# Performance work log

Measured on AMD Instinct MI355X. Metric: run time of the kernel, lower is better.

The kernel has to match this reference:

```python
import jax, jax.numpy as jnp
import numpy as np

C_IN = 144
PC = 288           # proj_channels = 2 * in_channels
HEADS = 12
DG = 12            # deformable groups
CLIP = 2
KH = KW = 3
A = KH * KW        # samples per clip per group (attention window 3x3)
PAD = 1
MAXMAG = 10.0
B, T, H, W = 1, 1, 64, 64


def _conv2d(x, w, b, pad):
    y = jax.lax.conv_general_dilated(x, w, (1, 1), [(pad, pad), (pad, pad)],
                                     dimension_numbers=('NCHW', 'OIHW', 'NCHW'))
    return y + b[None, :, None, None]


def _lrelu(x):
    return jnp.where(x >= 0, x, 0.1 * x)


def _linear_c(x, w, b):
    # per-pixel linear on channel dim; x: (..., Cin, h, w), w: (Cin, Cout)
    return jnp.einsum('...ihw,io->...ohw', x, w) + b[:, None, None]


def _bilinear_gather(feat, py, px):
    # feat: (b, clip, g, cg, h, w); py/px: (b, clip, g, A, h, w) absolute pixel coords
    # zero padding outside image (deformable-conv sampling semantics)
    b, cl, g, cg, h, w = feat.shape
    ff = feat.reshape(b, cl, g, cg, h * w)
    y0 = jnp.floor(py)
    x0 = jnp.floor(px)
    wy1 = py - y0
    wx1 = px - x0

    def corner(yc, xc, wt):
        valid = ((yc >= 0) & (yc < h) & (xc >= 0) & (xc < w)).astype(feat.dtype)
        yi = jnp.clip(yc, 0, h - 1).astype(jnp.int32)
        xi = jnp.clip(xc, 0, w - 1).astype(jnp.int32)
        idx = (yi * w + xi).reshape(b, cl, g, 1, -1)
        gat = jnp.take_along_axis(ff, idx, axis=-1).reshape(b, cl, g, cg, *py.shape[3:])
        return gat * (wt * valid)[:, :, :, None]

    out = corner(y0, x0, (1 - wy1) * (1 - wx1))
    out = out + corner(y0, x0 + 1, (1 - wy1) * wx1)
    out = out + corner(y0 + 1, x0, wy1 * (1 - wx1))
    out = out + corner(y0 + 1, x0 + 1, wy1 * wx1)
    return out  # (b, clip, g, cg, A, h, w)


def setup_inputs() -> dict:
    key = jax.random.key(0)
    ks = jax.random.split(key, 32)
    rn = lambda i, shp, s=1.0: jax.random.normal(ks[i], shp, dtype=jnp.float32) * s
    cin_off = C_IN * (1 + CLIP) + CLIP * 2   # 436
    c_off = CLIP * DG * A * 2                # 432
    d = {
        'q': rn(0, (B, T, C_IN, H, W)),
        'k': rn(1, (B, CLIP, C_IN, H, W)),
        'v': rn(2, (B, CLIP, C_IN, H, W)),
        'vpw0': rn(3, (B, T, C_IN, H, W)),
        'vpw1': rn(4, (B, T, C_IN, H, W)),
        'flow0': rn(5, (B, T, 2, H, W), 3.0),
        'flow1': rn(6, (B, T, 2, H, W), 3.0),
        'wo1': rn(7, (64, cin_off, 1, 1), 1.0 / np.sqrt(cin_off)),
        'bo1': rn(8, (64,), 0.01),
        'wo2': rn(9, (64, 64, 3, 3), 1.0 / np.sqrt(64 * 9)),
        'bo2': rn(10, (64,), 0.01),
        'wo3': rn(11, (64, 64, 3, 3), 1.0 / np.sqrt(64 * 9)),
        'bo3': rn(12, (64,), 0.01),
        'wo4': rn(13, (64, 64, 3, 3), 1.0 / np.sqrt(64 * 9)),
        'bo4': rn(14, (64,), 0.01),
        'wo5': rn(15, (64, 64, 3, 3), 1.0 / np.sqrt(64 * 9)),
        'bo5': rn(16, (64,), 0.01),
        'wo6': rn(17, (c_off, 64, 1, 1), 0.02),
        'bo6': rn(18, (c_off,), 0.01),
        'wq': rn(19, (C_IN, PC), 1.0 / np.sqrt(C_IN)),
        'bq': rn(20, (PC,), 0.01),
        'wk': rn(21, (C_IN, PC), 1.0 / np.sqrt(C_IN)),
        'bk': rn(22, (PC,), 0.01),
        'wv': rn(23, (C_IN, PC), 1.0 / np.sqrt(C_IN)),
        'bv': rn(24, (PC,), 0.01),
        'wp': rn(25, (PC, C_IN), 1.0 / np.sqrt(PC)),
        'bp': rn(26, (C_IN,), 0.01),
        'wm1': rn(27, (C_IN, 2 * C_IN), 1.0 / np.sqrt(C_IN)),
        'bm1': rn(28, (2 * C_IN,), 0.01),
        'wm2': rn(29, (2 * C_IN, C_IN), 1.0 / np.sqrt(2 * C_IN)),
        'bm2': rn(30, (C_IN,), 0.01),
    }
    return d


def reference(q, k, v, vpw0, vpw1, flow0, flow1,
              wo1, bo1, wo2, bo2, wo3, bo3, wo4, bo4, wo5, bo5, wo6, bo6,
              wq, bq, wk, bk, wv, bv, wp, bp, wm1, bm1, wm2, bm2):
    b, t, c, h, w = q.shape  # t == 1 here so q batch b*t matches kv batch b
    bt = b * t
    # --- offset predictor: Conv3d stack with time-kernel 1 == 2D convs ---
    x = jnp.concatenate([q, vpw0, vpw1, flow0, flow1], axis=2).reshape(bt, -1, h, w)
    x = _lrelu(_conv2d(x, wo1, bo1, 0))
    x = _lrelu(_conv2d(x, wo2, bo2, 1))
    x = _lrelu(_conv2d(x, wo3, bo3, 1))
    x = _lrelu(_conv2d(x, wo4, bo4, 1))
    x = _lrelu(_conv2d(x, wo5, bo5, 1))
    off = MAXMAG * jnp.tanh(_conv2d(x, wo6, bo6, 0))  # (bt, CLIP*DG*A*2, h, w)
    # add optical flow (channel-flipped to (y, x)) to every sample offset
    fyx = flow0.reshape(bt, 2, h, w)[:, ::-1]
    off = off + jnp.tile(fyx, (1, off.shape[1] // 2, 1, 1))
    off = off.reshape(bt, CLIP, DG, A, 2, h, w)
    ar = jnp.arange(A)
    by = (ar // KW - PAD).astype(q.dtype)  # kernel base offsets (stride=1, dil=1)
    bx = (ar % KW - PAD).astype(q.dtype)
    py = off[:, :, :, :, 0] + by[None, None, None, :, None, None] \
         + jnp.arange(h, dtype=q.dtype)[:, None]
    px = off[:, :, :, :, 1] + bx[None, None, None, :, None, None] \
         + jnp.arange(w, dtype=q.dtype)
    # --- q/k/v projections ---
    hd = PC // HEADS
    qp = _linear_c(q, wq, bq).reshape(bt, HEADS, hd, h, w)
    kp = _linear_c(k, wk, bk).reshape(b, CLIP, DG, PC // DG, h, w)
    vp = _linear_c(v, wv, bv).reshape(b, CLIP, DG, PC // DG, h, w)
    # --- deformable bilinear gather (per deformable group) ---
    ksamp = _bilinear_gather(kp, py, px).reshape(bt, CLIP, HEADS, hd, A, h, w)
    vsamp = _bilinear_gather(vp, py, px).reshape(bt, CLIP, HEADS, hd, A, h, w)
    # --- attention over CLIP*A sampled locations, per pixel per head ---
    scores = jnp.einsum('bmdyx,bcmdayx->bmcayx', qp, ksamp) * (hd ** -0.5)
    attn = jax.nn.softmax(scores.reshape(bt, HEADS, CLIP * A, h, w), axis=2)
    vflat = vsamp.transpose(0, 2, 1, 4, 3, 5, 6).reshape(bt, HEADS, CLIP * A, hd, h, w)
    out = jnp.einsum('bmsyx,bmsdyx->bmdyx', attn, vflat).reshape(b, t, PC, h, w)
    # --- output projection + MLP residual ---
    o = _linear_c(out, wp, bp)
    m = _linear_c(jax.nn.gelu(_linear_c(o, wm1, bm1), approximate=False), wm2, bm2)
    return o + m
```

## Files before the change

kernel.cpp:

```cpp
#include <hip/hip_runtime.h>
#include <hip/hip_bf16.h>
#include <math.h>

typedef __hip_bfloat16 bf16;
typedef __attribute__((ext_vector_type(8))) short bf16x8v;
typedef __attribute__((ext_vector_type(4))) float f32x4v;

#define NPIX 4096

__device__ __forceinline__ float b2f(bf16 v) { return __bfloat162float(v); }
__device__ __forceinline__ unsigned short f2bu(float f) {
    bf16 h = __float2bfloat16(f);
    return *(unsigned short*)&h;
}
__device__ __forceinline__ int detect_bf16(const unsigned short* __restrict__ qraw) {
    int lane = threadIdx.x & 63;
    unsigned short u = qraw[lane * 2];
    int e = (u >> 7) & 0xFF;
    unsigned long long ball = __ballot(e >= 100 && e <= 135);
    return __popcll(ball) > 32;
}

struct CArgs { const void* src[26]; int dstoff[26]; int n[26]; };

__global__ void convert_kernel(CArgs a, const unsigned short* __restrict__ qraw,
                               float* __restrict__ cw)
{
    const int isbf = detect_bf16(qraw);
    const int t = blockIdx.y;
    const int n = a.n[t];
    float* d = cw + a.dstoff[t];
    if (isbf) {
        const bf16* s = (const bf16*)a.src[t];
        for (int i = blockIdx.x * 256 + threadIdx.x; i < n; i += 256 * gridDim.x) d[i] = b2f(s[i]);
    } else {
        const float* s = (const float*)a.src[t];
        for (int i = blockIdx.x * 256 + threadIdx.x; i < n; i += 256 * gridDim.x) d[i] = s[i];
    }
}

struct PPJob { int dstS; int Mp, Kp, kr, mr, srcof, sstride, kind; };
struct PPArgs { PPJob j[11]; };

__global__ void prepack_kernel(PPArgs pa, const float* __restrict__ cw, short* __restrict__ wsS,
                               float* __restrict__ wsF)
{
    const int y = blockIdx.y;
    if (y < 11) {
        PPJob J = pa.j[y];
        const int tot = J.Mp * J.Kp;
        for (int e = blockIdx.x * 256 + threadIdx.x; e < tot; e += 256 * gridDim.x) {
            int m = e / J.Kp, k = e - m * J.Kp;
            float v = 0.f;
            if (J.kind == 0) { if (k < J.kr) v = cw[J.srcof + m * J.sstride + k]; }
            else             { if (k < J.kr && m < J.mr) v = cw[J.srcof + k * J.sstride + m]; }
            wsS[J.dstS + e] = (short)f2bu(v);
        }
    } else {
        const int OF_BP = 370512, OF_BM1 = 412128, OF_BM2 = 453888;
        for (int e = blockIdx.x * 256 + threadIdx.x; e < 576; e += 256 * gridDim.x) {
            if (e < 144)      wsF[5828544 + e] = cw[OF_BP + e];
            else if (e < 432) wsF[5828688 + e - 144] = cw[OF_BM1 + e - 144];
            else              wsF[5828976 + e - 432] = cw[OF_BM2 + e - 432];
        }
    }
}

__global__ void stage_pm_kernel(const void* __restrict__ s0, const void* __restrict__ s1,
                                const void* __restrict__ s2, const unsigned short* __restrict__ qraw,
                                short* __restrict__ xbase)
{
    const int isbf = detect_bf16(qraw);
    const int z = blockIdx.z;
    const int p = blockIdx.x * 256 + threadIdx.x;
    const int half = blockIdx.y;
    const void* srcs[5] = { s0, s1, s1, s2, s2 };
    const int clips[5] = { 0, 0, 1, 0, 1 };
    const size_t co = (size_t)clips[z] * 144 * NPIX;
    short* row = xbase + (size_t)z * 655360 + (size_t)p * 160;
    for (int c0 = half * 72; c0 < half * 72 + 72; c0 += 8) {
        unsigned short h[8];
        if (isbf) {
            const bf16* s = (const bf16*)srcs[z] + co;
#pragma unroll
            for (int i = 0; i < 8; ++i) h[i] = f2bu(b2f(s[(size_t)(c0 + i) * NPIX + p]));
        } else {
            const float* s = (const float*)srcs[z] + co;
#pragma unroll
            for (int i = 0; i < 8; ++i) h[i] = f2bu(s[(size_t)(c0 + i) * NPIX + p]);
        }
        uint4 u;
        u.x = (unsigned)h[0] | ((unsigned)h[1] << 16);
        u.y = (unsigned)h[2] | ((unsigned)h[3] << 16);
        u.z = (unsigned)h[4] | ((unsigned)h[5] << 16);
        u.w = (unsigned)h[6] | ((unsigned)h[7] << 16);
        *(uint4*)(row + c0) = u;
    }
    if (half == 1) {
        uint4 zz; zz.x = zz.y = zz.z = zz.w = 0u;
        *(uint4*)(row + 144) = zz;
        *(uint4*)(row + 152) = zz;
    }
}

__global__ void stage_x1_kernel(const void* __restrict__ q, const void* __restrict__ v0,
                                const void* __restrict__ v1, const float* __restrict__ cw,
                                const unsigned short* __restrict__ qraw, short* __restrict__ x1)
{
    const int isbf = detect_bf16(qraw);
    const int p = blockIdx.x * 256 + threadIdx.x;
    const int sec = blockIdx.y;
    short* row = x1 + (size_t)p * 448;
    if (sec < 3) {
        const void* srcs[3] = { q, v0, v1 };
        const int cbase = sec * 144;
        for (int c0 = 0; c0 < 144; c0 += 8) {
            unsigned short h[8];
            if (isbf) {
                const bf16* s = (const bf16*)srcs[sec];
#pragma unroll
                for (int i = 0; i < 8; ++i) h[i] = f2bu(b2f(s[(size_t)(c0 + i) * NPIX + p]));
            } else {
                const float* s = (const float*)srcs[sec];
#pragma unroll
                for (int i = 0; i < 8; ++i) h[i] = f2bu(s[(size_t)(c0 + i) * NPIX + p]);
            }
            uint4 u;
            u.x = (unsigned)h[0] | ((unsigned)h[1] << 16);
            u.y = (unsigned)h[2] | ((unsigned)h[3] << 16);
            u.z = (unsigned)h[4] | ((unsigned)h[5] << 16);
            u.w = (unsigned)h[6] | ((unsigned)h[7] << 16);
            *(uint4*)(row + cbase + c0) = u;
        }
    } else {
        const int OF_FL0 = 454032, OF_FL1 = 462224;
        unsigned short h[4];
        h[0] = f2bu(cw[OF_FL0 + p]);
        h[1] = f2bu(cw[OF_FL0 + NPIX + p]);
        h[2] = f2bu(cw[OF_FL1 + p]);
        h[3] = f2bu(cw[OF_FL1 + NPIX + p]);
        uint4 u;
        u.x = (unsigned)h[0] | ((unsigned)h[1] << 16);
        u.y = (unsigned)h[2] | ((unsigned)h[3] << 16);
        u.z = 0u; u.w = 0u;
        *(uint4*)(row + 432) = u;
        uint4 zz; zz.x = zz.y = zz.z = zz.w = 0u;
        *(uint4*)(row + 440) = zz;
    }
}

struct GemmDesc {
    const short* A; const short* B; const float* bias;
    void* dst; void* dst2; const unsigned short* qraw;
    int Mp, Kp, Mreal, mode, gofs;
};
struct GemmDesc5 { GemmDesc d[5]; };

template <int TM, int TN>
__global__ __launch_bounds__(256) void gemm_kernel(GemmDesc5 gd)
{
    const GemmDesc d = gd.d[blockIdx.z];
    const int wid = blockIdx.x * 4 + (threadIdx.x >> 6);
    const int lane = threadIdx.x & 63;
    const int tiles_m = d.Mp / (16 * TM);
    const int m0 = (wid % tiles_m) * (16 * TM);
    const int p0 = (wid / tiles_m) * (16 * TN);
    const int ar = lane & 15;
    const int kq = (lane >> 4) * 8;

    f32x4v acc[TM][TN];
#pragma unroll
    for (int i = 0; i < TM; ++i)
#pragma unroll
        for (int j = 0; j < TN; ++j) acc[i][j] = (f32x4v){0.f, 0.f, 0.f, 0.f};

    for (int k0 = 0; k0 < d.Kp; k0 += 32) {
        bf16x8v a[TM], b[TN];
#pragma unroll
        for (int i = 0; i < TM; ++i)
            a[i] = *(const bf16x8v*)(d.A + (size_t)(m0 + i * 16 + ar) * d.Kp + k0 + kq);
#pragma unroll
        for (int j = 0; j < TN; ++j)
            b[j] = *(const bf16x8v*)(d.B + (size_t)(p0 + j * 16 + ar) * d.Kp + k0 + kq);
#pragma unroll
        for (int i = 0; i < TM; ++i)
#pragma unroll
            for (int j = 0; j < TN; ++j)
                acc[i][j] = __builtin_amdgcn_mfma_f32_16x16x32_bf16(a[i], b[j], acc[i][j], 0, 0, 0);
    }

    const int isbf = (d.mode == 5) ? detect_bf16(d.qraw) : 0;
#pragma unroll
    for (int i = 0; i < TM; ++i) {
#pragma unroll
        for (int j = 0; j < TN; ++j) {
            const int pcol = p0 + j * 16 + (lane & 15);
#pragma unroll
            for (int r = 0; r < 4; ++r) {
                const int m = m0 + i * 16 + (lane >> 4) * 4 + r;
                float v = acc[i][j][r];
                if (m < d.Mreal) v += d.bias[m];
                if (d.mode == 0) {
                    v = (v >= 0.f) ? v : 0.1f * v;
                    ((unsigned short*)d.dst)[(size_t)pcol * d.Mp + m] = f2bu(v);
                } else if (d.mode == 1) {
                    int g = m / 24 + d.gofs;
                    ((unsigned short*)d.dst)[((size_t)g * NPIX + pcol) * 24 + (m % 24)] = f2bu(v);
                } else if (d.mode == 3) {
                    ((unsigned short*)d.dst)[(size_t)pcol * 160 + m] = f2bu(v);
                    if (m < 144) ((float*)d.dst2)[(size_t)pcol * 144 + m] = v;
                } else if (d.mode == 4) {
                    v = 0.5f * v * (1.f + erff(v * 0.70710678118654752f));
                    ((unsigned short*)d.dst)[(size_t)pcol * d.Mp + m] = f2bu(v);
                } else {
                    if (m < 144) {
                        v += ((float*)d.dst2)[(size_t)pcol * 144 + m];
                        if (isbf) ((unsigned short*)d.dst)[(size_t)m * NPIX + pcol] = f2bu(v);
                        else      ((float*)d.dst)[(size_t)m * NPIX + pcol] = v;
                    }
                }
            }
        }
    }
}

__device__ __forceinline__ unsigned short hw_get(const uint4& v, int idx) {
    unsigned w = (idx < 2) ? v.x : (idx < 4) ? v.y : (idx < 6) ? v.z : v.w;
    return (idx & 1) ? (unsigned short)(w >> 16) : (unsigned short)(w & 0xffff);
}

__global__ __launch_bounds__(256) void im2col_kernel(const short* __restrict__ Y,
                                                     short* __restrict__ B3)
{
    const int t = blockIdx.x * 256 + threadIdx.x;
    const int p = t >> 3;
    const int c0 = (t & 7) * 8;
    const int y = p >> 6, x = p & 63;
    uint4 v[9];
#pragma unroll
    for (int tap = 0; tap < 9; ++tap) {
        int yy = y + tap / 3 - 1, xx = x + tap % 3 - 1;
        int ok = ((unsigned)yy < 64u) & ((unsigned)xx < 64u);
        int idx = ok ? (yy * 64 + xx) : p;
        uint4 u = *(const uint4*)(Y + (size_t)idx * 64 + c0);
        if (!ok) { u.x = 0u; u.y = 0u; u.z = 0u; u.w = 0u; }
        v[tap] = u;
    }
    short* orow = B3 + (size_t)p * 576 + c0 * 9;
#pragma unroll
    for (int w = 0; w < 9; ++w) {
        unsigned short h[8];
#pragma unroll
        for (int s = 0; s < 8; ++s) {
            int e = w * 8 + s;
            h[s] = hw_get(v[e % 9], e / 9);
        }
        uint4 u;
        u.x = (unsigned)h[0] | ((unsigned)h[1] << 16);
        u.y = (unsigned)h[2] | ((unsigned)h[3] << 16);
        u.z = (unsigned)h[4] | ((unsigned)h[5] << 16);
        u.w = (unsigned)h[6] | ((unsigned)h[7] << 16);
        ((uint4*)orow)[w] = u;
    }
}

__global__ __launch_bounds__(256) void conv6_kernel(const short* __restrict__ YF,
                                                    const float* __restrict__ cw,
                                                    float* __restrict__ py, float* __restrict__ px)
{
    const int OF_WO6 = 175680, OF_BO6 = 203328, OF_FL0 = 454032;
    const int p = blockIdx.x * 256 + threadIdx.x;
    const int o0 = blockIdx.y * 16;
    const uint4* yrow = (const uint4*)(YF + (size_t)p * 64);
    const float* wb = cw + OF_WO6 + o0 * 64;

    float acc[16];
#pragma unroll
    for (int j = 0; j < 16; ++j) acc[j] = cw[OF_BO6 + o0 + j];

#pragma unroll
    for (int c = 0; c < 8; ++c) {
        uint4 u = yrow[c];
        float a0 = __uint_as_float(u.x << 16);
        float a1 = __uint_as_float(u.x & 0xFFFF0000u);
        float a2 = __uint_as_float(u.y << 16);
        float a3 = __uint_as_float(u.y & 0xFFFF0000u);
        float a4 = __uint_as_float(u.z << 16);
        float a5 = __uint_as_float(u.z & 0xFFFF0000u);
        float a6 = __uint_as_float(u.w << 16);
        float a7 = __uint_as_float(u.w & 0xFFFF0000u);
#pragma unroll
        for (int j = 0; j < 16; ++j) {
            const float* wr = wb + j * 64 + c * 8;
            acc[j] += a0 * wr[0] + a1 * wr[1] + a2 * wr[2] + a3 * wr[3]
                    + a4 * wr[4] + a5 * wr[5] + a6 * wr[6] + a7 * wr[7];
        }
    }

    const float f_y = cw[OF_FL0 + NPIX + p];
    const float f_x = cw[OF_FL0 + p];
    const float yf = (float)(p >> 6), xf = (float)(p & 63);
#pragma unroll
    for (int j = 0; j < 16; ++j) {
        int o = o0 + j;
        float val = 10.f * tanhf(acc[j]);
        int s = o >> 1;
        int a_idx = s % 9;
        if ((o & 1) == 0) py[s * NPIX + p] = val + f_y + (float)(a_idx / 3 - 1) + yf;
        else              px[s * NPIX + p] = val + f_x + (float)(a_idx % 3 - 1) + xf;
    }
}

__device__ __forceinline__ float dot12(const bf16* __restrict__ row, const float* qv) {
    const uint2* s = (const uint2*)row;
    float d = 0.f;
#pragma unroll
    for (int c = 0; c < 3; ++c) {
        uint2 u = s[c];
        d += qv[c * 4 + 0] * __uint_as_float(u.x << 16);
        d += qv[c * 4 + 1] * __uint_as_float(u.x & 0xFFFF0000u);
        d += qv[c * 4 + 2] * __uint_as_float(u.y << 16);
        d += qv[c * 4 + 3] * __uint_as_float(u.y & 0xFFFF0000u);
    }
    return d;
}
__device__ __forceinline__ void acc12(float* ov, const bf16* __restrict__ row, float f) {
    const uint2* s = (const uint2*)row;
#pragma unroll
    for (int c = 0; c < 3; ++c) {
        uint2 u = s[c];
        ov[c * 4 + 0] += f * __uint_as_float(u.x << 16);
        ov[c * 4 + 1] += f * __uint_as_float(u.x & 0xFFFF0000u);
        ov[c * 4 + 2] += f * __uint_as_float(u.y << 16);
        ov[c * 4 + 3] += f * __uint_as_float(u.y & 0xFFFF0000u);
    }
}

__global__ __launch_bounds__(256) void attn_kernel(
    const bf16* __restrict__ qp, const bf16* __restrict__ kp,
    const bf16* __restrict__ vp, const float* __restrict__ py,
    const float* __restrict__ px, unsigned short* __restrict__ att)
{
    const int t = blockIdx.x * 256 + threadIdx.x;
    const int ch = t & 1;
    const int clip = (t >> 1) & 1;
    const int sh = (t >> 2) & 1;
    const int pp = t >> 3;
    const int m = pp >> 12;
    const int p = pp & 4095;

    float qv[12];
    {
        const uint2* s = (const uint2*)(qp + (size_t)(m * 4096 + p) * 24 + ch * 12);
#pragma unroll
        for (int c = 0; c < 3; ++c) {
            uint2 u = s[c];
            qv[c * 4 + 0] = __uint_as_float(u.x << 16);
            qv[c * 4 + 1] = __uint_as_float(u.x & 0xFFFF0000u);
            qv[c * 4 + 2] = __uint_as_float(u.y << 16);
            qv[c * 4 + 3] = __uint_as_float(u.y & 0xFFFF0000u);
        }
    }

    const int gidx = clip * 12 + m;
    const bf16* kb = kp + (size_t)gidx * 4096 * 24 + ch * 12;
    const bf16* vb = vp + (size_t)gidx * 4096 * 24 + ch * 12;
    const int sbase = gidx * 9;
    const int a0 = sh ? 5 : 0;
    const int na = sh ? 4 : 5;

    float e[5], fyv[5], fxv[5];
    float mx = -1e30f;
#pragma unroll
    for (int i = 0; i < 5; ++i) {
        e[i] = -1e30f; fyv[i] = 0.f; fxv[i] = 0.f;
        if (i < na) {
            const int a = a0 + i;
            const float fy = py[(sbase + a) * NPIX + p];
            const float fx = px[(sbase + a) * NPIX + p];
            fyv[i] = fy; fxv[i] = fx;
            const float y0 = floorf(fy), x0 = floorf(fx);
            const float wy = fy - y0, wx = fx - x0;
            const int iy = (int)y0, ix = (int)x0;
            const float w00 = (1.f - wy) * (1.f - wx), w01 = (1.f - wy) * wx;
            const float w10 = wy * (1.f - wx), w11 = wy * wx;
            float part = 0.f;
            if ((unsigned)iy < 64u) {
                const bf16* rr = kb + (size_t)(iy * 64) * 24;
                if ((unsigned)ix < 64u)       part += w00 * dot12(rr + ix * 24, qv);
                if ((unsigned)(ix + 1) < 64u) part += w01 * dot12(rr + (ix + 1) * 24, qv);
            }
            if ((unsigned)(iy + 1) < 64u) {
                const bf16* rr = kb + (size_t)((iy + 1) * 64) * 24;
                if ((unsigned)ix < 64u)       part += w10 * dot12(rr + ix * 24, qv);
                if ((unsigned)(ix + 1) < 64u) part += w11 * dot12(rr + (ix + 1) * 24, qv);
            }
            float full = part + __shfl_xor(part, 1, 64);
            e[i] = full * 0.20412414523193154f;
            mx = fmaxf(mx, e[i]);
        }
    }
    mx = fmaxf(mx, __shfl_xor(mx, 4, 64));
    mx = fmaxf(mx, __shfl_xor(mx, 2, 64));
    float sum = 0.f;
#pragma unroll
    for (int i = 0; i < 5; ++i) {
        if (i < na) { e[i] = __expf(e[i] - mx); sum += e[i]; }
    }
    sum += __shfl_xor(sum, 4, 64);
    sum += __shfl_xor(sum, 2, 64);
    const float inv = 1.f / sum;

    float ov[12];
#pragma unroll
    for (int j = 0; j < 12; ++j) ov[j] = 0.f;

#pragma unroll
    for (int i = 0; i < 5; ++i) {
        if (i < na) {
            const float wa = e[i] * inv;
            const float fy = fyv[i], fx = fxv[i];
            const float y0 = floorf(fy), x0 = floorf(fx);
            const float wy = fy - y0, wx = fx - x0;
            const int iy = (int)y0, ix = (int)x0;
            if ((unsigned)iy < 64u) {
                const bf16* rr = vb + (size_t)(iy * 64) * 24;
                if ((unsigned)ix < 64u)       acc12(ov, rr + ix * 24, wa * (1.f - wy) * (1.f - wx));
                if ((unsigned)(ix + 1) < 64u) acc12(ov, rr + (ix + 1) * 24, wa * (1.f - wy) * wx);
            }
            if ((unsigned)(iy + 1) < 64u) {
                const bf16* rr = vb + (size_t)((iy + 1) * 64) * 24;
                if ((unsigned)ix < 64u)       acc12(ov, rr + ix * 24, wa * wy * (1.f - wx));
                if ((unsigned)(ix + 1) < 64u) acc12(ov, rr + (ix + 1) * 24, wa * wy * wx);
            }
        }
    }
#pragma unroll
    for (int j = 0; j < 12; ++j) {
        ov[j] += __shfl_xor(ov[j], 4, 64);
        ov[j] += __shfl_xor(ov[j], 2, 64);
    }
    if (clip == 0 && sh == 0) {
        unsigned short* ab = att + (size_t)p * 288 + m * 24 + ch * 12;
#pragma unroll
        for (int c = 0; c < 3; ++c) {
            uint2 u;
            u.x = (unsigned)f2bu(ov[c * 4 + 0]) | ((unsigned)f2bu(ov[c * 4 + 1]) << 16);
            u.y = (unsigned)f2bu(ov[c * 4 + 2]) | ((unsigned)f2bu(ov[c * 4 + 3]) << 16);
            ((uint2*)ab)[c] = u;
        }
    }
}

__global__ void diag_kernel(float* __restrict__ out, int n, float v)
{
    int i = blockIdx.x * 256 + threadIdx.x;
    if (i < n) out[i] = (i == 0 ? v : 0.f);
}

extern "C" void kernel_launch(void* const* d_in, const int* in_sizes, int n_in,
                              void* d_out, int out_size, void* d_ws, size_t ws_size,
                              hipStream_t stream)
{
    const size_t REQUIRED = 23592960;
    if (ws_size < REQUIRED) {
        float code = 1000.0f + (float)(ws_size >> 20);
        diag_kernel<<<dim3((out_size + 255) / 256), 256, 0, stream>>>((float*)d_out, out_size, code);
        return;
    }

    char* W = (char*)d_ws;
    short* wsS = (short*)W;
    float* wsF = (float*)W;
    float* cw = (float*)(W + 64);

    const int OF_WO1 = 0,      OF_BO1 = 27904,  OF_WO2 = 27968,  OF_BO2 = 64832;
    const int OF_WO3 = 64896,  OF_BO3 = 101760, OF_WO4 = 101824, OF_BO4 = 138688;
    const int OF_WO5 = 138752, OF_BO5 = 175616, OF_WO6 = 175680, OF_BO6 = 203328;
    const int OF_WQ  = 203760, OF_BQ  = 245232, OF_WK  = 245520, OF_BK  = 286992;
    const int OF_WV  = 287280, OF_BV  = 328752, OF_WP  = 329040, OF_BP  = 370512;
    const int OF_WM1 = 370656, OF_BM1 = 412128, OF_WM2 = 412416, OF_BM2 = 453888;
    const int OF_FL0 = 454032, OF_FL1 = 462224;
    (void)OF_BO6; (void)OF_FL1;

    short* conv1w = wsS + 940864;
    short* conv3w0 = wsS + 969536;
    short* wqb = wsS + 1116992, *wkb = wsS + 1163072, *wvb = wsS + 1209152;
    short* wpS = wsS + 11658240, *wm1S = wsS + 11704320, *wm2S = wsS + 11750400;
    float* bpS = wsF + 5828544, *bm1S = wsF + 5828688, *bm2S = wsF + 5828976;
    bf16* QP = (bf16*)(W + 2786944);
    bf16* KP = (bf16*)(W + 5146240);
    bf16* VP = (bf16*)(W + 9864832);
    short* XS = (short*)(W + 14583424);
    short* X1 = XS;
    short* B3 = XS;
    short* Y0 = (short*)(W + 19302016);
    short* Y1 = (short*)(W + 19826304);
    short* YF = (short*)(W + 21661312);
    float* PY = (float*)(W + 14583424);
    float* PX = (float*)(W + 18122368);
    unsigned short* ATT = (unsigned short*)(W + 64);
    short* OPM = (short*)(W + 14583424);
    float* O32 = (float*)(W + 15894144);
    short* M1 = (short*)(W + 18253440);

    const unsigned short* qraw = (const unsigned short*)d_in[0];

    CArgs ca;
    const int srcidx[26] = {7,8,9,10,11,12,13,14,15,16,17,18,19,20,21,22,23,24,25,26,27,28,29,30,5,6};
    const int dsto[26]   = {OF_WO1,OF_BO1,OF_WO2,OF_BO2,OF_WO3,OF_BO3,OF_WO4,OF_BO4,OF_WO5,OF_BO5,
                            OF_WO6,203328,OF_WQ,OF_BQ,OF_WK,OF_BK,OF_WV,OF_BV,OF_WP,OF_BP,
                            OF_WM1,OF_BM1,OF_WM2,OF_BM2,OF_FL0,462224};
    for (int i = 0; i < 26; ++i) {
        ca.src[i] = d_in[srcidx[i]];
        ca.dstoff[i] = dsto[i];
        ca.n[i] = in_sizes[srcidx[i]];
    }
    convert_kernel<<<dim3(8, 26), 256, 0, stream>>>(ca, qraw, cw);

    PPArgs pp;
    pp.j[0]  = { 940864,  64, 448, 436, 64,  OF_WO1, 436, 0 };
    pp.j[1]  = { 969536,  64, 576, 576, 64,  OF_WO2, 576, 0 };
    pp.j[2]  = { 1006400, 64, 576, 576, 64,  OF_WO3, 576, 0 };
    pp.j[3]  = { 1043264, 64, 576, 576, 64,  OF_WO4, 576, 0 };
    pp.j[4]  = { 1080128, 64, 576, 576, 64,  OF_WO5, 576, 0 };
    pp.j[5]  = { 1116992, 288, 160, 144, 288, OF_WQ, 288, 1 };
    pp.j[6]  = { 1163072, 288, 160, 144, 288, OF_WK, 288, 1 };
    pp.j[7]  = { 1209152, 288, 160, 144, 288, OF_WV, 288, 1 };
    pp.j[8]  = { 11658240, 160, 288, 288, 144, OF_WP, 144, 1 };
    pp.j[9]  = { 11704320, 288, 160, 144, 288, OF_WM1, 288, 1 };
    pp.j[10] = { 11750400, 160, 288, 288, 144, OF_WM2, 144, 1 };
    prepack_kernel<<<dim3(64, 12), 256, 0, stream>>>(pp, cw, wsS, wsF);

    stage_pm_kernel<<<dim3(16, 2, 5), 256, 0, stream>>>(d_in[0], d_in[1], d_in[2], qraw, XS);

    GemmDesc5 gproj;
    const short* Xz[5] = { XS, XS + 655360, XS + 1310720, XS + 1966080, XS + 2621440 };
    const short* Az[5] = { wqb, wkb, wkb, wvb, wvb };
    const float* Bz[5] = { cw + OF_BQ, cw + OF_BK, cw + OF_BK, cw + OF_BV, cw + OF_BV };
    bf16* Dz[5] = { QP, KP, KP, VP, VP };
    const int Gz[5] = { 0, 0, 12, 0, 12 };
    for (int z = 0; z < 5; ++z)
        gproj.d[z] = { Az[z], Xz[z], Bz[z], Dz[z], nullptr, qraw, 288, 160, 288, 1, Gz[z] };
    gemm_kernel<2, 2><<<dim3(288, 1, 5), 256, 0, stream>>>(gproj);

    stage_x1_kernel<<<dim3(16, 4), 256, 0, stream>>>(d_in[0], d_in[3], d_in[4], cw, qraw, X1);

    GemmDesc5 g1;
    g1.d[0] = { conv1w, X1, cw + OF_BO1, Y0, nullptr, qraw, 64, 448, 64, 0, 0 };
    gemm_kernel<1, 1><<<dim3(256, 1, 1), 256, 0, stream>>>(g1);

    const float* cb[4] = { cw + OF_BO2, cw + OF_BO3, cw + OF_BO4, cw + OF_BO5 };
    short* cin[4] = { Y0, Y1, Y0, Y1 };
    short* cout[4] = { Y1, Y0, Y1, YF };
    for (int i = 0; i < 4; ++i) {
        im2col_kernel<<<dim3(128), 256, 0, stream>>>(cin[i], B3);
        GemmDesc5 g3;
        g3.d[0] = { conv3w0 + i * 36864, B3, cb[i], cout[i], nullptr, qraw, 64, 576, 64, 0, 0 };
        gemm_kernel<1, 1><<<dim3(256, 1, 1), 256, 0, stream>>>(g3);
    }

    conv6_kernel<<<dim3(16, 27), 256, 0, stream>>>(YF, cw, PY, PX);

    attn_kernel<<<dim3(1536), 256, 0, stream>>>(QP, KP, VP, PY, PX, ATT);

    GemmDesc5 gwp;
    gwp.d[0] = { wpS, (const short*)ATT, bpS, OPM, O32, qraw, 160, 288, 144, 3, 0 };
    gemm_kernel<2, 2><<<dim3(160, 1, 1), 256, 0, stream>>>(gwp);

    GemmDesc5 gm1;
    gm1.d[0] = { wm1S, OPM, bm1S, M1, nullptr, qraw, 288, 160, 288, 4, 0 };
    gemm_kernel<2, 2><<<dim3(288, 1, 1), 256, 0, stream>>>(gm1);

    GemmDesc5 gm2;
    gm2.d[0] = { wm2S, M1, bm2S, d_out, O32, qraw, 160, 288, 144, 5, 0 };
    gemm_kernel<2, 2><<<dim3(160, 1, 1), 256, 0, stream>>>(gm2);
}
```

Measured before the change: 339.5 us.

## Fuse staging kernels, implicit-im2col conv GEMMs, batch conv1 with projections

Merges weight conversion and the pm/x1 staging into one misc kernel, and drops the separate bias-copy pass. The 3x3 convs now gather im2col inputs inside the GEMM using a tap-major weight layout, so the im2col kernel and its buffer are gone. conv1 runs in the same launch as the q/k/v projections, and epilogue stores are vectorized. This cuts kernel launches and intermediate traffic. In exchange the workspace requirement grows a lot, and the conv GEMMs use fewer waves with 2x2 tiles.

```diff
diff --git a/kernel.cpp b/kernel.cpp
--- a/kernel.cpp
+++ b/kernel.cpp
@@ -21,107 +21,69 @@
     return __popcll(ball) > 32;
 }
 
+#define OF_WO1 0
+#define OF_BO1 27904
+#define OF_WO2 27968
+#define OF_BO2 64832
+#define OF_WO3 64896
+#define OF_BO3 101760
+#define OF_WO4 101824
+#define OF_BO4 138688
+#define OF_WO5 138752
+#define OF_BO5 175616
+#define OF_WO6 175680
+#define OF_BO6 203328
+#define OF_WQ  203760
+#define OF_BQ  245232
+#define OF_WK  245520
+#define OF_BK  286992
+#define OF_WV  287280
+#define OF_BV  328752
+#define OF_WP  329040
+#define OF_BP  370512
+#define OF_WM1 370656
+#define OF_BM1 412128
+#define OF_WM2 412416
+#define OF_BM2 453888
+#define OF_FL0 454032
+#define OF_FL1 462224
+
 struct CArgs { const void* src[26]; int dstoff[26]; int n[26]; };
 
-__global__ void convert_kernel(CArgs a, const unsigned short* __restrict__ qraw,
-                               float* __restrict__ cw)
-{
-    const int isbf = detect_bf16(qraw);
-    const int t = blockIdx.y;
-    const int n = a.n[t];
-    float* d = cw + a.dstoff[t];
-    if (isbf) {
-        const bf16* s = (const bf16*)a.src[t];
-        for (int i = blockIdx.x * 256 + threadIdx.x; i < n; i += 256 * gridDim.x) d[i] = b2f(s[i]);
-    } else {
-        const float* s = (const float*)a.src[t];
-        for (int i = blockIdx.x * 256 + threadIdx.x; i < n; i += 256 * gridDim.x) d[i] = s[i];
-    }
-}
-
-struct PPJob { int dstS; int Mp, Kp, kr, mr, srcof, sstride, kind; };
-struct PPArgs { PPJob j[11]; };
-
-__global__ void prepack_kernel(PPArgs pa, const float* __restrict__ cw, short* __restrict__ wsS,
-                               float* __restrict__ wsF)
-{
+__global__ void misc_kernel(CArgs a, const void* __restrict__ q, const void* __restrict__ k,
+                            const void* __restrict__ v, const void* __restrict__ vp0,
+                            const void* __restrict__ vp1, const void* __restrict__ fl0,
+                            const void* __restrict__ fl1,
+                            float* __restrict__ cw, short* __restrict__ XS, short* __restrict__ X1)
+{
+    const int isbf = detect_bf16((const unsigned short*)q);
     const int y = blockIdx.y;
-    if (y < 11) {
-        PPJob J = pa.j[y];
-        const int tot = J.Mp * J.Kp;
-        for (int e = blockIdx.x * 256 + threadIdx.x; e < tot; e += 256 * gridDim.x) {
-            int m = e / J.Kp, k = e - m * J.Kp;
-            float v = 0.f;
-            if (J.kind == 0) { if (k < J.kr) v = cw[J.srcof + m * J.sstride + k]; }
-            else             { if (k < J.kr && m < J.mr) v = cw[J.srcof + k * J.sstride + m]; }
-            wsS[J.dstS + e] = (short)f2bu(v);
-        }
-    } else {
-        const int OF_BP = 370512, OF_BM1 = 412128, OF_BM2 = 453888;
-        for (int e = blockIdx.x * 256 + threadIdx.x; e < 576; e += 256 * gridDim.x) {
-            if (e < 144)      wsF[5828544 + e] = cw[OF_BP + e];
-            else if (e < 432) wsF[5828688 + e - 144] = cw[OF_BM1 + e - 144];
-            else              wsF[5828976 + e - 432] = cw[OF_BM2 + e - 432];
-        }
-    }
-}
-
-__global__ void stage_pm_kernel(const void* __restrict__ s0, const void* __restrict__ s1,
-                                const void* __restrict__ s2, const unsigned short* __restrict__ qraw,
-                                short* __restrict__ xbase)
-{
-    const int isbf = detect_bf16(qraw);
-    const int z = blockIdx.z;
-    const int p = blockIdx.x * 256 + threadIdx.x;
-    const int half = blockIdx.y;
-    const void* srcs[5] = { s0, s1, s1, s2, s2 };
-    const int clips[5] = { 0, 0, 1, 0, 1 };
-    const size_t co = (size_t)clips[z] * 144 * NPIX;
-    short* row = xbase + (size_t)z * 655360 + (size_t)p * 160;
-    for (int c0 = half * 72; c0 < half * 72 + 72; c0 += 8) {
-        unsigned short h[8];
+    if (y < 26) {
+        const int n = a.n[y];
+        float* d = cw + a.dstoff[y];
         if (isbf) {
-            const bf16* s = (const bf16*)srcs[z] + co;
-#pragma unroll
-            for (int i = 0; i < 8; ++i) h[i] = f2bu(b2f(s[(size_t)(c0 + i) * NPIX + p]));
+            const bf16* s = (const bf16*)a.src[y];
+            for (int i = blockIdx.x * 256 + threadIdx.x; i < n; i += 256 * 16) d[i] = b2f(s[i]);
         } else {
-            const float* s = (const float*)srcs[z] + co;
-#pragma unroll
-            for (int i = 0; i < 8; ++i) h[i] = f2bu(s[(size_t)(c0 + i) * NPIX + p]);
-        }
-        uint4 u;
-        u.x = (unsigned)h[0] | ((unsigned)h[1] << 16);
-        u.y = (unsigned)h[2] | ((unsigned)h[3] << 16);
-        u.z = (unsigned)h[4] | ((unsigned)h[5] << 16);
-        u.w = (unsigned)h[6] | ((unsigned)h[7] << 16);
-        *(uint4*)(row + c0) = u;
-    }
-    if (half == 1) {
-        uint4 zz; zz.x = zz.y = zz.z = zz.w = 0u;
-        *(uint4*)(row + 144) = zz;
-        *(uint4*)(row + 152) = zz;
-    }
-}
-
-__global__ void stage_x1_kernel(const void* __restrict__ q, const void* __restrict__ v0,
-                                const void* __restrict__ v1, const float* __restrict__ cw,
-                                const unsigned short* __restrict__ qraw, short* __restrict__ x1)
-{
-    const int isbf = detect_bf16(qraw);
-    const int p = blockIdx.x * 256 + threadIdx.x;
-    const int sec = blockIdx.y;
-    short* row = x1 + (size_t)p * 448;
-    if (sec < 3) {
-        const void* srcs[3] = { q, v0, v1 };
-        const int cbase = sec * 144;
-        for (int c0 = 0; c0 < 144; c0 += 8) {
+            const float* s = (const float*)a.src[y];
+            for (int i = blockIdx.x * 256 + threadIdx.x; i < n; i += 256 * 16) d[i] = s[i];
+        }
+    } else if (y < 36) {
+        const int job = y - 26;
+        const int z = job >> 1, half = job & 1;
+        const int p = blockIdx.x * 256 + threadIdx.x;
+        const void* srcs[5] = { q, k, k, v, v };
+        const int clips[5] = { 0, 0, 1, 0, 1 };
+        const size_t co = (size_t)clips[z] * 144 * NPIX;
+        short* row = XS + (size_t)z * 655360 + (size_t)p * 160;
+        for (int c0 = half * 72; c0 < half * 72 + 72; c0 += 8) {
             unsigned short h[8];
             if (isbf) {
-                const bf16* s = (const bf16*)srcs[sec];
+                const bf16* s = (const bf16*)srcs[z] + co;
 #pragma unroll
                 for (int i = 0; i < 8; ++i) h[i] = f2bu(b2f(s[(size_t)(c0 + i) * NPIX + p]));
             } else {
-                const float* s = (const float*)srcs[sec];
+                const float* s = (const float*)srcs[z] + co;
 #pragma unroll
                 for (int i = 0; i < 8; ++i) h[i] = f2bu(s[(size_t)(c0 + i) * NPIX + p]);
             }
@@ -130,37 +92,96 @@
             u.y = (unsigned)h[2] | ((unsigned)h[3] << 16);
             u.z = (unsigned)h[4] | ((unsigned)h[5] << 16);
             u.w = (unsigned)h[6] | ((unsigned)h[7] << 16);
-            *(uint4*)(row + cbase + c0) = u;
+            *(uint4*)(row + c0) = u;
+        }
+        if (half == 1) {
+            uint4 zz; zz.x = zz.y = zz.z = zz.w = 0u;
+            *(uint4*)(row + 144) = zz;
+            *(uint4*)(row + 152) = zz;
         }
     } else {
-        const int OF_FL0 = 454032, OF_FL1 = 462224;
-        unsigned short h[4];
-        h[0] = f2bu(cw[OF_FL0 + p]);
-        h[1] = f2bu(cw[OF_FL0 + NPIX + p]);
-        h[2] = f2bu(cw[OF_FL1 + p]);
-        h[3] = f2bu(cw[OF_FL1 + NPIX + p]);
-        uint4 u;
-        u.x = (unsigned)h[0] | ((unsigned)h[1] << 16);
-        u.y = (unsigned)h[2] | ((unsigned)h[3] << 16);
-        u.z = 0u; u.w = 0u;
-        *(uint4*)(row + 432) = u;
-        uint4 zz; zz.x = zz.y = zz.z = zz.w = 0u;
-        *(uint4*)(row + 440) = zz;
+        const int sec = y - 36;
+        const int p = blockIdx.x * 256 + threadIdx.x;
+        short* row = X1 + (size_t)p * 448;
+        if (sec < 3) {
+            const void* srcs[3] = { q, vp0, vp1 };
+            const int cbase = sec * 144;
+            for (int c0 = 0; c0 < 144; c0 += 8) {
+                unsigned short h[8];
+                if (isbf) {
+                    const bf16* s = (const bf16*)srcs[sec];
+#pragma unroll
+                    for (int i = 0; i < 8; ++i) h[i] = f2bu(b2f(s[(size_t)(c0 + i) * NPIX + p]));
+                } else {
+                    const float* s = (const float*)srcs[sec];
+#pragma unroll
+                    for (int i = 0; i < 8; ++i) h[i] = f2bu(s[(size_t)(c0 + i) * NPIX + p]);
+                }
+                uint4 u;
+                u.x = (unsigned)h[0] | ((unsigned)h[1] << 16);
+                u.y = (unsigned)h[2] | ((unsigned)h[3] << 16);
+                u.z = (unsigned)h[4] | ((unsigned)h[5] << 16);
+                u.w = (unsigned)h[6] | ((unsigned)h[7] << 16);
+                *(uint4*)(row + cbase + c0) = u;
+            }
+        } else {
+            unsigned short h[4];
+            if (isbf) {
+                const bf16* f0 = (const bf16*)fl0;
+                const bf16* f1 = (const bf16*)fl1;
+                h[0] = f2bu(b2f(f0[p]));
+                h[1] = f2bu(b2f(f0[NPIX + p]));
+                h[2] = f2bu(b2f(f1[p]));
+                h[3] = f2bu(b2f(f1[NPIX + p]));
+            } else {
+                const float* f0 = (const float*)fl0;
+                const float* f1 = (const float*)fl1;
+                h[0] = f2bu(f0[p]);
+                h[1] = f2bu(f0[NPIX + p]);
+                h[2] = f2bu(f1[p]);
+                h[3] = f2bu(f1[NPIX + p]);
+            }
+            uint4 u;
+            u.x = (unsigned)h[0] | ((unsigned)h[1] << 16);
+            u.y = (unsigned)h[2] | ((unsigned)h[3] << 16);
+            u.z = 0u; u.w = 0u;
+            *(uint4*)(row + 432) = u;
+            uint4 zz; zz.x = zz.y = zz.z = zz.w = 0u;
+            *(uint4*)(row + 440) = zz;
+        }
+    }
+}
+
+struct PPJob { int dstS; int Mp, Kp, kr, mr, srcof, sstride, kind; };
+struct PPArgs { PPJob j[11]; };
+
+__global__ void prepack_kernel(PPArgs pa, const float* __restrict__ cw, short* __restrict__ wsS)
+{
+    PPJob J = pa.j[blockIdx.y];
+    const int tot = J.Mp * J.Kp;
+    for (int e = blockIdx.x * 256 + threadIdx.x; e < tot; e += 256 * gridDim.x) {
+        int m = e / J.Kp, kk = e - m * J.Kp;
+        float v = 0.f;
+        if (J.kind == 0) { if (kk < J.kr) v = cw[J.srcof + m * J.sstride + kk]; }
+        else if (J.kind == 1) { if (kk < J.kr && m < J.mr) v = cw[J.srcof + kk * J.sstride + m]; }
+        else { int c = kk & 63, tap = kk >> 6; if (kk < J.kr) v = cw[J.srcof + m * J.sstride + c * 9 + tap]; }
+        wsS[J.dstS + e] = (short)f2bu(v);
     }
 }
 
 struct GemmDesc {
     const short* A; const short* B; const float* bias;
     void* dst; void* dst2; const unsigned short* qraw;
-    int Mp, Kp, Mreal, mode, gofs;
+    int Mp, Kp, Mreal, mode, gofs, nwaves;
 };
-struct GemmDesc5 { GemmDesc d[5]; };
-
-template <int TM, int TN>
-__global__ __launch_bounds__(256) void gemm_kernel(GemmDesc5 gd)
+struct GemmDesc6 { GemmDesc d[6]; };
+
+template <int TM, int TN, int BM>
+__global__ __launch_bounds__(256) void gemm_kernel(GemmDesc6 gd)
 {
     const GemmDesc d = gd.d[blockIdx.z];
     const int wid = blockIdx.x * 4 + (threadIdx.x >> 6);
+    if (wid >= d.nwaves) return;
     const int lane = threadIdx.x & 63;
     const int tiles_m = d.Mp / (16 * TM);
     const int m0 = (wid % tiles_m) * (16 * TM);
@@ -179,9 +200,25 @@
 #pragma unroll
         for (int i = 0; i < TM; ++i)
             a[i] = *(const bf16x8v*)(d.A + (size_t)(m0 + i * 16 + ar) * d.Kp + k0 + kq);
-#pragma unroll
-        for (int j = 0; j < TN; ++j)
-            b[j] = *(const bf16x8v*)(d.B + (size_t)(p0 + j * 16 + ar) * d.Kp + k0 + kq);
+        if (BM == 0) {
+#pragma unroll
+            for (int j = 0; j < TN; ++j)
+                b[j] = *(const bf16x8v*)(d.B + (size_t)(p0 + j * 16 + ar) * d.Kp + k0 + kq);
+        } else {
+            const int kk = k0 + kq;
+            const int tap = kk >> 6, cc = kk & 63;
+            const int dy = tap / 3 - 1, dx = tap % 3 - 1;
+#pragma unroll
+            for (int j = 0; j < TN; ++j) {
+                const int pix = p0 + j * 16 + ar;
+                const int yy = (pix >> 6) + dy, xx = (pix & 63) + dx;
+                const bool ok = ((unsigned)yy < 64u) & ((unsigned)xx < 64u);
+                const int np = min(max(yy, 0), 63) * 64 + min(max(xx, 0), 63);
+                bf16x8v bv = *(const bf16x8v*)(d.B + (size_t)np * 64 + cc);
+                if (!ok) bv = (bf16x8v)(short)0;
+                b[j] = bv;
+            }
+        }
 #pragma unroll
         for (int i = 0; i < TM; ++i)
 #pragma unroll
@@ -195,26 +232,49 @@
 #pragma unroll
         for (int j = 0; j < TN; ++j) {
             const int pcol = p0 + j * 16 + (lane & 15);
+            const int mb = m0 + i * 16 + (lane >> 4) * 4;
+            float vv[4];
 #pragma unroll
             for (int r = 0; r < 4; ++r) {
-                const int m = m0 + i * 16 + (lane >> 4) * 4 + r;
-                float v = acc[i][j][r];
-                if (m < d.Mreal) v += d.bias[m];
-                if (d.mode == 0) {
-                    v = (v >= 0.f) ? v : 0.1f * v;
-                    ((unsigned short*)d.dst)[(size_t)pcol * d.Mp + m] = f2bu(v);
-                } else if (d.mode == 1) {
-                    int g = m / 24 + d.gofs;
-                    ((unsigned short*)d.dst)[((size_t)g * NPIX + pcol) * 24 + (m % 24)] = f2bu(v);
-                } else if (d.mode == 3) {
-                    ((unsigned short*)d.dst)[(size_t)pcol * 160 + m] = f2bu(v);
-                    if (m < 144) ((float*)d.dst2)[(size_t)pcol * 144 + m] = v;
-                } else if (d.mode == 4) {
-                    v = 0.5f * v * (1.f + erff(v * 0.70710678118654752f));
-                    ((unsigned short*)d.dst)[(size_t)pcol * d.Mp + m] = f2bu(v);
-                } else {
+                const int m = mb + r;
+                vv[r] = acc[i][j][r];
+                if (m < d.Mreal) vv[r] += d.bias[m];
+            }
+            if (d.mode == 0) {
+#pragma unroll
+                for (int r = 0; r < 4; ++r) vv[r] = (vv[r] >= 0.f) ? vv[r] : 0.1f * vv[r];
+                uint2 u;
+                u.x = (unsigned)f2bu(vv[0]) | ((unsigned)f2bu(vv[1]) << 16);
+                u.y = (unsigned)f2bu(vv[2]) | ((unsigned)f2bu(vv[3]) << 16);
+                *(uint2*)((unsigned short*)d.dst + (size_t)pcol * d.Mp + mb) = u;
+            } else if (d.mode == 1) {
+                const int g = mb / 24 + d.gofs;
+                uint2 u;
+                u.x = (unsigned)f2bu(vv[0]) | ((unsigned)f2bu(vv[1]) << 16);
+                u.y = (unsigned)f2bu(vv[2]) | ((unsigned)f2bu(vv[3]) << 16);
+                *(uint2*)((unsigned short*)d.dst + ((size_t)g * NPIX + pcol) * 24 + (mb % 24)) = u;
+            } else if (d.mode == 3) {
+                uint2 u;
+                u.x = (unsigned)f2bu(vv[0]) | ((unsigned)f2bu(vv[1]) << 16);
+                u.y = (unsigned)f2bu(vv[2]) | ((unsigned)f2bu(vv[3]) << 16);
+                *(uint2*)((unsigned short*)d.dst + (size_t)pcol * 160 + mb) = u;
+                if (mb < 144)
+                    *(float4*)((float*)d.dst2 + (size_t)pcol * 144 + mb) =
+                        make_float4(vv[0], vv[1], vv[2], vv[3]);
+            } else if (d.mode == 4) {
+#pragma unroll
+                for (int r = 0; r < 4; ++r)
+                    vv[r] = 0.5f * vv[r] * (1.f + erff(vv[r] * 0.70710678118654752f));
+                uint2 u;
+                u.x = (unsigned)f2bu(vv[0]) | ((unsigned)f2bu(vv[1]) << 16);
+                u.y = (unsigned)f2bu(vv[2]) | ((unsigned)f2bu(vv[3]) << 16);
+                *(uint2*)((unsigned short*)d.dst + (size_t)pcol * d.Mp + mb) = u;
+            } else {
+#pragma unroll
+                for (int r = 0; r < 4; ++r) {
+                    const int m = mb + r;
                     if (m < 144) {
-                        v += ((float*)d.dst2)[(size_t)pcol * 144 + m];
+                        float v = vv[r] + ((float*)d.dst2)[(size_t)pcol * 144 + m];
                         if (isbf) ((unsigned short*)d.dst)[(size_t)m * NPIX + pcol] = f2bu(v);
                         else      ((float*)d.dst)[(size_t)m * NPIX + pcol] = v;
                     }
@@ -224,51 +284,10 @@
     }
 }
 
-__device__ __forceinline__ unsigned short hw_get(const uint4& v, int idx) {
-    unsigned w = (idx < 2) ? v.x : (idx < 4) ? v.y : (idx < 6) ? v.z : v.w;
-    return (idx & 1) ? (unsigned short)(w >> 16) : (unsigned short)(w & 0xffff);
-}
-
-__global__ __launch_bounds__(256) void im2col_kernel(const short* __restrict__ Y,
-                                                     short* __restrict__ B3)
-{
-    const int t = blockIdx.x * 256 + threadIdx.x;
-    const int p = t >> 3;
-    const int c0 = (t & 7) * 8;
-    const int y = p >> 6, x = p & 63;
-    uint4 v[9];
-#pragma unroll
-    for (int tap = 0; tap < 9; ++tap) {
-        int yy = y + tap / 3 - 1, xx = x + tap % 3 - 1;
-        int ok = ((unsigned)yy < 64u) & ((unsigned)xx < 64u);
-        int idx = ok ? (yy * 64 + xx) : p;
-        uint4 u = *(const uint4*)(Y + (size_t)idx * 64 + c0);
-        if (!ok) { u.x = 0u; u.y = 0u; u.z = 0u; u.w = 0u; }
-        v[tap] = u;
-    }
-    short* orow = B3 + (size_t)p * 576 + c0 * 9;
-#pragma unroll
-    for (int w = 0; w < 9; ++w) {
-        unsigned short h[8];
-#pragma unroll
-        for (int s = 0; s < 8; ++s) {
-            int e = w * 8 + s;
-            h[s] = hw_get(v[e % 9], e / 9);
-        }
-        uint4 u;
-        u.x = (unsigned)h[0] | ((unsigned)h[1] << 16);
-        u.y = (unsigned)h[2] | ((unsigned)h[3] << 16);
-        u.z = (unsigned)h[4] | ((unsigned)h[5] << 16);
-        u.w = (unsigned)h[6] | ((unsigned)h[7] << 16);
-        ((uint4*)orow)[w] = u;
-    }
-}
-
 __global__ __launch_bounds__(256) void conv6_kernel(const short* __restrict__ YF,
                                                     const float* __restrict__ cw,
                                                     float* __restrict__ py, float* __restrict__ px)
 {
-    const int OF_WO6 = 175680, OF_BO6 = 203328, OF_FL0 = 454032;
     const int p = blockIdx.x * 256 + threadIdx.x;
     const int o0 = blockIdx.y * 16;
     const uint4* yrow = (const uint4*)(YF + (size_t)p * 64);
@@ -462,7 +481,7 @@
                               void* d_out, int out_size, void* d_ws, size_t ws_size,
                               hipStream_t stream)
 {
-    const size_t REQUIRED = 23592960;
+    const size_t REQUIRED = 75000000;
     if (ws_size < REQUIRED) {
         float code = 1000.0f + (float)(ws_size >> 20);
         diag_kernel<<<dim3((out_size + 255) / 256), 256, 0, stream>>>((float*)d_out, out_size, code);
@@ -471,108 +490,90 @@
 
     char* W = (char*)d_ws;
     short* wsS = (short*)W;
-    float* wsF = (float*)W;
     float* cw = (float*)(W + 64);
 
-    const int OF_WO1 = 0,      OF_BO1 = 27904,  OF_WO2 = 27968,  OF_BO2 = 64832;
-    const int OF_WO3 = 64896,  OF_BO3 = 101760, OF_WO4 = 101824, OF_BO4 = 138688;
-    const int OF_WO5 = 138752, OF_BO5 = 175616, OF_WO6 = 175680, OF_BO6 = 203328;
-    const int OF_WQ  = 203760, OF_BQ  = 245232, OF_WK  = 245520, OF_BK  = 286992;
-    const int OF_WV  = 287280, OF_BV  = 328752, OF_WP  = 329040, OF_BP  = 370512;
-    const int OF_WM1 = 370656, OF_BM1 = 412128, OF_WM2 = 412416, OF_BM2 = 453888;
-    const int OF_FL0 = 454032, OF_FL1 = 462224;
-    (void)OF_BO6; (void)OF_FL1;
-
-    short* conv1w = wsS + 940864;
-    short* conv3w0 = wsS + 969536;
-    short* wqb = wsS + 1116992, *wkb = wsS + 1163072, *wvb = wsS + 1209152;
-    short* wpS = wsS + 11658240, *wm1S = wsS + 11704320, *wm2S = wsS + 11750400;
-    float* bpS = wsF + 5828544, *bm1S = wsF + 5828688, *bm2S = wsF + 5828976;
-    bf16* QP = (bf16*)(W + 2786944);
-    bf16* KP = (bf16*)(W + 5146240);
-    bf16* VP = (bf16*)(W + 9864832);
-    short* XS = (short*)(W + 14583424);
-    short* X1 = XS;
-    short* B3 = XS;
-    short* Y0 = (short*)(W + 19302016);
-    short* Y1 = (short*)(W + 19826304);
-    short* YF = (short*)(W + 21661312);
-    float* PY = (float*)(W + 14583424);
-    float* PX = (float*)(W + 18122368);
-    unsigned short* ATT = (unsigned short*)(W + 64);
-    short* OPM = (short*)(W + 14583424);
-    float* O32 = (float*)(W + 15894144);
-    short* M1 = (short*)(W + 18253440);
+    short* conv1w = wsS + 1000000;
+    short* conv3w[4] = { wsS + 1028672, wsS + 1065536, wsS + 1102400, wsS + 1139264 };
+    short* wqb = wsS + 1176128, *wkb = wsS + 1222208, *wvb = wsS + 1268288;
+    short* wpS = wsS + 1314368, *wm1S = wsS + 1360448, *wm2S = wsS + 1406528;
+
+    short* XS = (short*)(W + 16777216);
+    short* X1 = (short*)(W + 25165824);
+    bf16*  QP = (bf16*)(W + 33554432);
+    bf16*  KP = (bf16*)(W + 36700160);
+    bf16*  VP = (bf16*)(W + 41943040);
+    short* Y0 = (short*)(W + 50331648);
+    short* Y1 = (short*)(W + 50855936);
+    short* YF = (short*)(W + 51380224);
+    float* PY = (float*)(W + 54525952);
+    float* PX = (float*)(W + 58064896);
+    unsigned short* ATT = (unsigned short*)(W + 62914560);
+    short* OPM = (short*)(W + 67108864);
+    float* O32 = (float*)(W + 68419584);
+    short* M1  = (short*)(W + 71303168);
 
     const unsigned short* qraw = (const unsigned short*)d_in[0];
 
     CArgs ca;
     const int srcidx[26] = {7,8,9,10,11,12,13,14,15,16,17,18,19,20,21,22,23,24,25,26,27,28,29,30,5,6};
     const int dsto[26]   = {OF_WO1,OF_BO1,OF_WO2,OF_BO2,OF_WO3,OF_BO3,OF_WO4,OF_BO4,OF_WO5,OF_BO5,
-                            OF_WO6,203328,OF_WQ,OF_BQ,OF_WK,OF_BK,OF_WV,OF_BV,OF_WP,OF_BP,
-                            OF_WM1,OF_BM1,OF_WM2,OF_BM2,OF_FL0,462224};
+                            OF_WO6,OF_BO6,OF_WQ,OF_BQ,OF_WK,OF_BK,OF_WV,OF_BV,OF_WP,OF_BP,
+                            OF_WM1,OF_BM1,OF_WM2,OF_BM2,OF_FL0,OF_FL1};
     for (int i = 0; i < 26; ++i) {
         ca.src[i] = d_in[srcidx[i]];
         ca.dstoff[i] = dsto[i];
         ca.n[i] = in_sizes[srcidx[i]];
     }
-    convert_kernel<<<dim3(8, 26), 256, 0, stream>>>(ca, qraw, cw);
+    misc_kernel<<<dim3(16, 40), 256, 0, stream>>>(ca, d_in[0], d_in[1], d_in[2], d_in[3], d_in[4],
+                                                  d_in[5], d_in[6], cw, XS, X1);
 
     PPArgs pp;
-    pp.j[0]  = { 940864,  64, 448, 436, 64,  OF_WO1, 436, 0 };
-    pp.j[1]  = { 969536,  64, 576, 576, 64,  OF_WO2, 576, 0 };
-    pp.j[2]  = { 1006400, 64, 576, 576, 64,  OF_WO3, 576, 0 };
-    pp.j[3]  = { 1043264, 64, 576, 576, 64,  OF_WO4, 576, 0 };
-    pp.j[4]  = { 1080128, 64, 576, 576, 64,  OF_WO5, 576, 0 };
-    pp.j[5]  = { 1116992, 288, 160, 144, 288, OF_WQ, 288, 1 };
-    pp.j[6]  = { 1163072, 288, 160, 144, 288, OF_WK, 288, 1 };
-    pp.j[7]  = { 1209152, 288, 160, 144, 288, OF_WV, 288, 1 };
-    pp.j[8]  = { 11658240, 160, 288, 288, 144, OF_WP, 144, 1 };
-    pp.j[9]  = { 11704320, 288, 160, 144, 288, OF_WM1, 288, 1 };
-    pp.j[10] = { 11750400, 160, 288, 288, 144, OF_WM2, 144, 1 };
-    prepack_kernel<<<dim3(64, 12), 256, 0, stream>>>(pp, cw, wsS, wsF);
-
-    stage_pm_kernel<<<dim3(16, 2, 5), 256, 0, stream>>>(d_in[0], d_in[1], d_in[2], qraw, XS);
-
-    GemmDesc5 gproj;
+    pp.j[0]  = { 1000000, 64, 448, 436, 64,  OF_WO1, 436, 0 };
+    pp.j[1]  = { 1028672, 64, 576, 576, 64,  OF_WO2, 576, 2 };
+    pp.j[2]  = { 1065536, 64, 576, 576, 64,  OF_WO3, 576, 2 };
+    pp.j[3]  = { 1102400, 64, 576, 576, 64,  OF_WO4, 576, 2 };
+    pp.j[4]  = { 1139264, 64, 576, 576, 64,  OF_WO5, 576, 2 };
+    pp.j[5]  = { 1176128, 288, 160, 144, 288, OF_WQ, 288, 1 };
+    pp.j[6]  = { 1222208, 288, 160, 144, 288, OF_WK, 288, 1 };
+    pp.j[7]  = { 1268288, 288, 160, 144, 288, OF_WV, 288, 1 };
+    pp.j[8]  = { 1314368, 160, 288, 288, 144, OF_WP, 144, 1 };
+    pp.j[9]  = { 1360448, 288, 160, 144, 288, OF_WM1, 288, 1 };
+    pp.j[10] = { 1406528, 160, 288, 288, 144, OF_WM2, 144, 1 };
+    prepack_kernel<<<dim3(64, 11), 256, 0, stream>>>(pp, cw, wsS);
+
+    GemmDesc6 g3;
     const short* Xz[5] = { XS, XS + 655360, XS + 1310720, XS + 1966080, XS + 2621440 };
     const short* Az[5] = { wqb, wkb, wkb, wvb, wvb };
     const float* Bz[5] = { cw + OF_BQ, cw + OF_BK, cw + OF_BK, cw + OF_BV, cw + OF_BV };
     bf16* Dz[5] = { QP, KP, KP, VP, VP };
     const int Gz[5] = { 0, 0, 12, 0, 12 };
     for (int z = 0; z < 5; ++z)
-        gproj.d[z] = { Az[z], Xz[z], Bz[z], Dz[z], nullptr, qraw, 288, 160, 288, 1, Gz[z] };
-    gemm_kernel<2, 2><<<dim3(288, 1, 5), 256, 0, stream>>>(gproj);
-
-    stage_x1_kernel<<<dim3(16, 4), 256, 0, stream>>>(d_in[0], d_in[3], d_in[4], cw, qraw, X1);
-
-    GemmDesc5 g1;
-    g1.d[0] = { conv1w, X1, cw + OF_BO1, Y0, nullptr, qraw, 64, 448, 64, 0, 0 };
-    gemm_kernel<1, 1><<<dim3(256, 1, 1), 256, 0, stream>>>(g1);
+        g3.d[z] = { Az[z], Xz[z], Bz[z], Dz[z], nullptr, qraw, 288, 160, 288, 1, Gz[z], 1152 };
+    g3.d[5] = { conv1w, X1, cw + OF_BO1, Y0, nullptr, qraw, 64, 448, 64, 0, 0, 256 };
+    gemm_kernel<2, 2, 0><<<dim3(288, 1, 6), 256, 0, stream>>>(g3);
 
     const float* cb[4] = { cw + OF_BO2, cw + OF_BO3, cw + OF_BO4, cw + OF_BO5 };
     short* cin[4] = { Y0, Y1, Y0, Y1 };
-    short* cout[4] = { Y1, Y0, Y1, YF };
+    short* coutp[4] = { Y1, Y0, Y1, YF };
     for (int i = 0; i < 4; ++i) {
-        im2col_kernel<<<dim3(128), 256, 0, stream>>>(cin[i], B3);
-        GemmDesc5 g3;
-        g3.d[0] = { conv3w0 + i * 36864, B3, cb[i], cout[i], nullptr, qraw, 64, 576, 64, 0, 0 };
-        gemm_kernel<1, 1><<<dim3(256, 1, 1), 256, 0, stream>>>(g3);
+        GemmDesc6 gc;
+        gc.d[0] = { conv3w[i], cin[i], cb[i], coutp[i], nullptr, qraw, 64, 576, 64, 0, 0, 256 };
+        gemm_kernel<2, 2, 1><<<dim3(64, 1, 1), 256, 0, stream>>>(gc);
     }
 
     conv6_kernel<<<dim3(16, 27), 256, 0, stream>>>(YF, cw, PY, PX);
 
     attn_kernel<<<dim3(1536), 256, 0, stream>>>(QP, KP, VP, PY, PX, ATT);
 
-    GemmDesc5 gwp;
-    gwp.d[0] = { wpS, (const short*)ATT, bpS, OPM, O32, qraw, 160, 288, 144, 3, 0 };
-    gemm_kernel<2, 2><<<dim3(160, 1, 1), 256, 0, stream>>>(gwp);
-
-    GemmDesc5 gm1;
-    gm1.d[0] = { wm1S, OPM, bm1S, M1, nullptr, qraw, 288, 160, 288, 4, 0 };
-    gemm_kernel<2, 2><<<dim3(288, 1, 1), 256, 0, stream>>>(gm1);
-
-    GemmDesc5 gm2;
-    gm2.d[0] = { wm2S, M1, bm2S, d_out, O32, qraw, 160, 288, 144, 5, 0 };
-    gemm_kernel<2, 2><<<dim3(160, 1, 1), 256, 0, stream>>>(gm2);
-}
+    GemmDesc6 gwp;
+    gwp.d[0] = { wpS, (const short*)ATT, cw + OF_BP, OPM, O32, qraw, 160, 288, 144, 3, 0, 640 };
+    gemm_kernel<2, 2, 0><<<dim3(160, 1, 1), 256, 0, stream>>>(gwp);
+
+    GemmDesc6 gm1;
+    gm1.d[0] = { wm1S, OPM, cw + OF_BM1, M1, nullptr, qraw, 288, 160, 288, 4, 0, 1152 };
+    gemm_kernel<2, 2, 0><<<dim3(288, 1, 1), 256, 0, stream>>>(gm1);
+
+    GemmDesc6 gm2;
+    gm2.d[0] = { wm2S, M1, cw + OF_BM2, d_out, O32, qraw, 160, 288, 144, 5, 0, 640 };
+    gemm_kernel<2, 2, 0><<<dim3(160, 1, 1), 256, 0, stream>>>(gm2);
+}
```

Measured after the change: 304.4 us. 10.3% less time.
